# Kernel tuning notes

Measured on AMD Instinct MI355X. Metric: run time of the kernel, lower is better.

Reference implementation:

```python
import jax, jax.numpy as jnp
import numpy as np

N_BLOCKS = 16
BLOCK_SIZE = 512
TOP_K = N_BLOCKS // 4  # matches n_blocks // 4 in the source


def setup_inputs() -> dict:
    key = jax.random.key(0)
    k1, k2, k3, k4, k5 = jax.random.split(key, 5)
    in_f, out_f = 2048, 8192
    x = jax.random.normal(k1, (2, 4096, in_f), dtype=jnp.float32)
    # router: Linear(in_features, n_blocks)
    Wr = jax.random.normal(k2, (N_BLOCKS, in_f), dtype=jnp.float32) * (in_f ** -0.5)
    br = jnp.zeros((N_BLOCKS,), dtype=jnp.float32)
    # fc1: Linear(in, out); fc2: Linear(out, in). Biases are unused in the original forward.
    W1 = jax.random.normal(k3, (out_f, in_f), dtype=jnp.float32) * (in_f ** -0.5)
    W2 = jax.random.normal(k4, (in_f, out_f), dtype=jnp.float32) * (out_f ** -0.5)
    return {"x": x, "Wr": Wr, "br": br, "W1": W1, "W2": W2}


def reference(x, Wr, br, W1, W2):
    x_shape = x.shape
    in_f = x_shape[-1]
    xf = x.reshape(-1, in_f)                      # [N, in]
    n = xf.shape[0]
    # router + top-k block selection per token
    prob = jax.nn.softmax(xf @ Wr.T + br, axis=-1)          # [N, nb]
    _, idx = jax.lax.top_k(prob, TOP_K)                      # [N, k]
    mask = jnp.zeros((n, N_BLOCKS), dtype=xf.dtype)
    mask = mask.at[jnp.arange(n)[:, None], idx].set(1.0)     # [N, nb]
    # fc1 per block: h[n,i,b] = x @ W1_block_i^T  (bias never used in source)
    W1b = W1.reshape(N_BLOCKS, BLOCK_SIZE, in_f)
    h = jnp.einsum('nf,ibf->nib', xf, W1b)                   # [N, nb, bs]
    # activation, then zero out unselected blocks (unselected never reach fc2)
    h = jax.nn.gelu(h, approximate=False) * mask[:, :, None]
    # fc2 per block accumulate: y = sum_i h_i @ W2_block_i^T
    W2b = W2.reshape(in_f, N_BLOCKS, BLOCK_SIZE)
    y = jnp.einsum('nib,fib->nf', h, W2b)                    # [N, in]
    return y.reshape(x_shape)
```

## Files before the change

### kernel.cpp

```cpp
#include <hip/hip_runtime.h>
#include <hip/hip_bf16.h>

#define N_TOK 8192
#define IN_F  2048
#define OUT_F 8192
#define NB    16
#define BS    512
#define BM    128
#define MAX_MT 272

typedef short          bf16x8  __attribute__((ext_vector_type(8)));
typedef unsigned short ushort8 __attribute__((ext_vector_type(8)));
typedef float          f32x4   __attribute__((ext_vector_type(4)));
typedef _Float16       f16x8   __attribute__((ext_vector_type(8)));

#define WS_COUNTS 0
#define WS_TSTART 64
#define WS_SEL    256
#define WS_INV    (32*1024)
#define WS_LISTS  (192*1024)
#define WS_XBF    (1ull<<20)
#define WS_W1BF   (WS_XBF + 33554432ull)
#define WS_W2BF   WS_XBF
#define WS_H      (WS_XBF + 67108864ull)
#define WS_YP     (WS_H + 35651584ull)

static __device__ __forceinline__ unsigned short f2bf(float f) {
    __hip_bfloat16 h = __float2bfloat16(f);
    return *reinterpret_cast<unsigned short*>(&h);
}

static __device__ __forceinline__ void gload16(const unsigned short* g, unsigned short* lds) {
    __builtin_amdgcn_global_load_lds(
        (const __attribute__((address_space(1))) unsigned int*)g,
        (__attribute__((address_space(3))) unsigned int*)lds, 16, 0, 0);
}

__global__ __launch_bounds__(256) void router_kernel(
    const float* __restrict__ x, const float* __restrict__ Wr,
    const float* __restrict__ br, unsigned short* __restrict__ sel)
{
    const int tid = threadIdx.x;
    const int lt = tid & 63;
    const int wv = tid >> 6;
    const int tok = blockIdx.x * 4 + wv;
    const int e = lt >> 2, p = lt & 3;
    const float4* xp = (const float4*)(x + (size_t)tok * IN_F);
    const float4* wp = (const float4*)(Wr + (size_t)e * IN_F);
    double s = 0.0;
    for (int j = p; j < IN_F / 4; j += 4) {
        float4 a = xp[j], w = wp[j];
        s += (double)a.x * w.x + (double)a.y * w.y + (double)a.z * w.z + (double)a.w * w.w;
    }
    s += __shfl_down(s, 2);
    s += __shfl_down(s, 1);
    __shared__ double logits[4][NB];
    if (p == 0) logits[wv][e] = s + (double)br[e];
    __syncthreads();
    if (lt == 0) {
        unsigned used = 0, packed = 0;
        #pragma unroll
        for (int kk = 0; kk < 4; ++kk) {
            int best = 0; double bv = -1.0e300;
            #pragma unroll
            for (int i = 0; i < NB; ++i)
                if (!((used >> i) & 1u) && logits[wv][i] > bv) { bv = logits[wv][i]; best = i; }
            used |= 1u << best;
            packed |= (unsigned)best << (4 * kk);
        }
        sel[tok] = (unsigned short)packed;
    }
}

__global__ __launch_bounds__(256) void build_lists_kernel(
    const unsigned short* __restrict__ sel, int* __restrict__ counts,
    int* __restrict__ lists, unsigned* __restrict__ inv)
{
    const int e = blockIdx.x;
    const int t = threadIdx.x;
    unsigned short mysel[N_TOK / 256];
    int cnt = 0;
    #pragma unroll
    for (int i = 0; i < N_TOK / 256; ++i) {
        unsigned s = sel[i * 256 + t];
        mysel[i] = (unsigned short)s;
        bool m = ((s & 15u) == (unsigned)e) | (((s >> 4) & 15u) == (unsigned)e) |
                 (((s >> 8) & 15u) == (unsigned)e) | (((s >> 12) & 15u) == (unsigned)e);
        cnt += m ? 1 : 0;
    }
    __shared__ int ps[256];
    ps[t] = cnt;
    __syncthreads();
    #pragma unroll
    for (int off = 1; off < 256; off <<= 1) {
        int v = (t >= off) ? ps[t - off] : 0;
        __syncthreads();
        ps[t] += v;
        __syncthreads();
    }
    int pos = ps[t] - cnt;
    if (t == 255) counts[e] = ps[255];
    #pragma unroll
    for (int i = 0; i < N_TOK / 256; ++i) {
        unsigned s = mysel[i];
        bool m = ((s & 15u) == (unsigned)e) | (((s >> 4) & 15u) == (unsigned)e) |
                 (((s >> 8) & 15u) == (unsigned)e) | (((s >> 12) & 15u) == (unsigned)e);
        if (m) {
            const int tok = i * 256 + t;
            int j = ((s & 15u) == (unsigned)e) ? 0 :
                    (((s >> 4) & 15u) == (unsigned)e) ? 1 :
                    (((s >> 8) & 15u) == (unsigned)e) ? 2 : 3;
            inv[tok * 4 + j] = ((unsigned)e << 16) | (unsigned)pos;
            lists[e * N_TOK + pos++] = tok;
        }
    }
}

__global__ void scan_kernel(const int* __restrict__ counts, int* __restrict__ tstart)
{
    if (threadIdx.x == 0) {
        int acc = 0;
        for (int i = 0; i < NB; ++i) { tstart[i] = acc; acc += (counts[i] + BM - 1) / BM; }
        tstart[NB] = acc;
    }
}

__global__ __launch_bounds__(256) void convert_swz_kernel(
    const float* __restrict__ src, unsigned short* __restrict__ dst, int sh)
{
    const int total = 1 << 21;
    for (int id = blockIdx.x * 256 + threadIdx.x; id < total; id += 2048 * 256) {
        const int row = id >> sh;
        const int sr  = id & ((1 << sh) - 1);
        const int ps  = sr ^ (row & 7);
        const float4* s4 = (const float4*)(src + ((size_t)id << 3));
        float4 p0 = s4[0], p1 = s4[1];
        ushort8 o;
        o[0] = f2bf(p0.x); o[1] = f2bf(p0.y); o[2] = f2bf(p0.z); o[3] = f2bf(p0.w);
        o[4] = f2bf(p1.x); o[5] = f2bf(p1.y); o[6] = f2bf(p1.z); o[7] = f2bf(p1.w);
        *(ushort8*)(dst + (((size_t)(row) << sh) << 3) + ((size_t)ps << 3)) = o;
    }
}

__global__ __launch_bounds__(256) void fc1_kernel(
    const unsigned short* __restrict__ x_bf, const unsigned short* __restrict__ w1_bf,
    const int* __restrict__ lists, const int* __restrict__ counts,
    const int* __restrict__ tstart, unsigned short* __restrict__ h)
{
    __shared__ unsigned short As[2][BM * 64];
    __shared__ unsigned short Bs[2][BM * 64];
    const int bid = blockIdx.x;
    const int newid = (bid & 7) * 136 + (bid >> 3);
    const int nt = newid & 3, mt = newid >> 2;
    if (mt >= tstart[NB]) return;
    int b = 0;
    #pragma unroll
    for (int i = 1; i < NB; ++i) b += (mt >= tstart[i]);
    const int cnt  = counts[b];
    const int row0 = (mt - tstart[b]) * BM;
    const int tid  = threadIdx.x;
    const int wave = tid >> 6, lane = tid & 63;
    const int sr8 = lane >> 3, sph = lane & 7;

    const unsigned short* aS[4];
    const unsigned short* bS[4];
    const int loff = wave * 2048;
    #pragma unroll
    for (int t = 0; t < 4; ++t) {
        const int r = wave * 32 + t * 8 + sr8;
        const int gr = min(row0 + r, cnt - 1);
        const int tok = lists[b * N_TOK + gr];
        aS[t] = x_bf + (size_t)tok * IN_F + ((sph ^ sr8 ^ (tok & 7)) << 3);
        bS[t] = w1_bf + (size_t)(b * BS + nt * BM + r) * IN_F + (sph << 3);
    }

    const int lr16 = lane & 15, q = lane >> 4;
    const int wm = (wave >> 1) * 64, wn = (wave & 1) * 64;
    int offA[4], offB[4];
    #pragma unroll
    for (int i = 0; i < 4; ++i) {
        const int r = wm + i * 16 + lr16;
        offA[i] = r * 64 + ((q ^ (r & 7)) << 3);
    }
    #pragma unroll
    for (int j = 0; j < 4; ++j) {
        const int r = wn + j * 16 + lr16;
        offB[j] = r * 64 + ((q ^ (r & 7)) << 3);
    }

    f32x4 acc[4][4];
    #pragma unroll
    for (int i = 0; i < 4; ++i)
        #pragma unroll
        for (int j = 0; j < 4; ++j) acc[i][j] = (f32x4)0.0f;

    #pragma unroll
    for (int t = 0; t < 4; ++t) {
        gload16(aS[t], &As[0][loff + t * 512]);
        gload16(bS[t], &Bs[0][loff + t * 512]);
    }
    __syncthreads();

    const int NK = IN_F / 64;
    for (int k = 0; k < NK; ++k) {
        const int cur = k & 1;
        if (k + 1 < NK) {
            const int ko = (k + 1) * 64;
            #pragma unroll
            for (int t = 0; t < 4; ++t) {
                gload16(aS[t] + ko, &As[cur ^ 1][loff + t * 512]);
                gload16(bS[t] + ko, &Bs[cur ^ 1][loff + t * 512]);
            }
        }
        #pragma unroll
        for (int kk = 0; kk < 2; ++kk) {
            const int kx = kk << 5;
            bf16x8 a0 = *(const bf16x8*)&As[cur][offA[0] ^ kx];
            bf16x8 a1 = *(const bf16x8*)&As[cur][offA[1] ^ kx];
            bf16x8 a2 = *(const bf16x8*)&As[cur][offA[2] ^ kx];
            bf16x8 a3 = *(const bf16x8*)&As[cur][offA[3] ^ kx];
            bf16x8 b0 = *(const bf16x8*)&Bs[cur][offB[0] ^ kx];
            bf16x8 b1 = *(const bf16x8*)&Bs[cur][offB[1] ^ kx];
            bf16x8 b2 = *(const bf16x8*)&Bs[cur][offB[2] ^ kx];
            bf16x8 b3 = *(const bf16x8*)&Bs[cur][offB[3] ^ kx];
            acc[0][0] = __builtin_amdgcn_mfma_f32_16x16x32_bf16(a0, b0, acc[0][0], 0, 0, 0);
            acc[0][1] = __builtin_amdgcn_mfma_f32_16x16x32_bf16(a0, b1, acc[0][1], 0, 0, 0);
            acc[0][2] = __builtin_amdgcn_mfma_f32_16x16x32_bf16(a0, b2, acc[0][2], 0, 0, 0);
            acc[0][3] = __builtin_amdgcn_mfma_f32_16x16x32_bf16(a0, b3, acc[0][3], 0, 0, 0);
            acc[1][0] = __builtin_amdgcn_mfma_f32_16x16x32_bf16(a1, b0, acc[1][0], 0, 0, 0);
            acc[1][1] = __builtin_amdgcn_mfma_f32_16x16x32_bf16(a1, b1, acc[1][1], 0, 0, 0);
            acc[1][2] = __builtin_amdgcn_mfma_f32_16x16x32_bf16(a1, b2, acc[1][2], 0, 0, 0);
            acc[1][3] = __builtin_amdgcn_mfma_f32_16x16x32_bf16(a1, b3, acc[1][3], 0, 0, 0);
            acc[2][0] = __builtin_amdgcn_mfma_f32_16x16x32_bf16(a2, b0, acc[2][0], 0, 0, 0);
            acc[2][1] = __builtin_amdgcn_mfma_f32_16x16x32_bf16(a2, b1, acc[2][1], 0, 0, 0);
            acc[2][2] = __builtin_amdgcn_mfma_f32_16x16x32_bf16(a2, b2, acc[2][2], 0, 0, 0);
            acc[2][3] = __builtin_amdgcn_mfma_f32_16x16x32_bf16(a2, b3, acc[2][3], 0, 0, 0);
            acc[3][0] = __builtin_amdgcn_mfma_f32_16x16x32_bf16(a3, b0, acc[3][0], 0, 0, 0);
            acc[3][1] = __builtin_amdgcn_mfma_f32_16x16x32_bf16(a3, b1, acc[3][1], 0, 0, 0);
            acc[3][2] = __builtin_amdgcn_mfma_f32_16x16x32_bf16(a3, b2, acc[3][2], 0, 0, 0);
            acc[3][3] = __builtin_amdgcn_mfma_f32_16x16x32_bf16(a3, b3, acc[3][3], 0, 0, 0);
        }
        __syncthreads();
    }
    #pragma unroll
    for (int i = 0; i < 4; ++i) {
        #pragma unroll
        for (int r = 0; r < 4; ++r) {
            const int lrow = wm + i * 16 + q * 4 + r;
            if (row0 + lrow < cnt) {
                const size_t hrow = (size_t)(mt * BM + lrow) * BS;
                const int r7 = (lrow & 7) << 3;
                #pragma unroll
                for (int j = 0; j < 4; ++j) {
                    const int col = nt * BM + wn + j * 16 + lr16;
                    float v = acc[i][j][r];
                    v = 0.5f * v * (1.0f + erff(v * 0.70710678118654752f));
                    h[hrow + (col ^ r7)] = f2bf(v);
                }
            }
        }
    }
}

__global__ __launch_bounds__(256) void fc2_kernel(
    const unsigned short* __restrict__ h, const unsigned short* __restrict__ w2_bf,
    const int* __restrict__ counts, const int* __restrict__ tstart,
    _Float16* __restrict__ yp)
{
    __shared__ unsigned short As[2][BM * 64];
    __shared__ unsigned short Bs[2][BM * 64];
    const int bid = blockIdx.x;
    const int newid = (bid & 7) * 544 + (bid >> 3);
    const int nt = newid & 15, mt = newid >> 4;
    if (mt >= tstart[NB]) return;
    int b = 0;
    #pragma unroll
    for (int i = 1; i < NB; ++i) b += (mt >= tstart[i]);
    const int cnt  = counts[b];
    const int row0 = (mt - tstart[b]) * BM;
    const int tid  = threadIdx.x;
    const int wave = tid >> 6, lane = tid & 63;
    const int sr8 = lane >> 3, sph = lane & 7;

    const unsigned short* aS[4];
    const unsigned short* bS[4];
    const int loff = wave * 2048;
    #pragma unroll
    for (int t = 0; t < 4; ++t) {
        const int r = wave * 32 + t * 8 + sr8;
        aS[t] = h + (size_t)(mt * BM + r) * BS + (sph << 3);
        bS[t] = w2_bf + (size_t)(nt * BM + r) * OUT_F + b * BS + (sph << 3);
    }

    const int lr16 = lane & 15, q = lane >> 4;
    const int wm = (wave >> 1) * 64, wn = (wave & 1) * 64;
    int offA[4], offB[4];
    #pragma unroll
    for (int i = 0; i < 4; ++i) {
        const int r = wm + i * 16 + lr16;
        offA[i] = r * 64 + ((q ^ (r & 7)) << 3);
    }
    #pragma unroll
    for (int j = 0; j < 4; ++j) {
        const int r = wn + j * 16 + lr16;
        offB[j] = r * 64 + ((q ^ (r & 7)) << 3);
    }

    f32x4 acc[4][4];
    #pragma unroll
    for (int i = 0; i < 4; ++i)
        #pragma unroll
        for (int j = 0; j < 4; ++j) acc[i][j] = (f32x4)0.0f;

    #pragma unroll
    for (int t = 0; t < 4; ++t) {
        gload16(aS[t], &As[0][loff + t * 512]);
        gload16(bS[t], &Bs[0][loff + t * 512]);
    }
    __syncthreads();

    const int NK = BS / 64;
    for (int k = 0; k < NK; ++k) {
        const int cur = k & 1;
        if (k + 1 < NK) {
            const int ko = (k + 1) * 64;
            #pragma unroll
            for (int t = 0; t < 4; ++t) {
                gload16(aS[t] + ko, &As[cur ^ 1][loff + t * 512]);
                gload16(bS[t] + ko, &Bs[cur ^ 1][loff + t * 512]);
            }
        }
        #pragma unroll
        for (int kk = 0; kk < 2; ++kk) {
            const int kx = kk << 5;
            bf16x8 a0 = *(const bf16x8*)&As[cur][offA[0] ^ kx];
            bf16x8 a1 = *(const bf16x8*)&As[cur][offA[1] ^ kx];
            bf16x8 a2 = *(const bf16x8*)&As[cur][offA[2] ^ kx];
            bf16x8 a3 = *(const bf16x8*)&As[cur][offA[3] ^ kx];
            bf16x8 b0 = *(const bf16x8*)&Bs[cur][offB[0] ^ kx];
            bf16x8 b1 = *(const bf16x8*)&Bs[cur][offB[1] ^ kx];
            bf16x8 b2 = *(const bf16x8*)&Bs[cur][offB[2] ^ kx];
            bf16x8 b3 = *(const bf16x8*)&Bs[cur][offB[3] ^ kx];
            acc[0][0] = __builtin_amdgcn_mfma_f32_16x16x32_bf16(a0, b0, acc[0][0], 0, 0, 0);
            acc[0][1] = __builtin_amdgcn_mfma_f32_16x16x32_bf16(a0, b1, acc[0][1], 0, 0, 0);
            acc[0][2] = __builtin_amdgcn_mfma_f32_16x16x32_bf16(a0, b2, acc[0][2], 0, 0, 0);
            acc[0][3] = __builtin_amdgcn_mfma_f32_16x16x32_bf16(a0, b3, acc[0][3], 0, 0, 0);
            acc[1][0] = __builtin_amdgcn_mfma_f32_16x16x32_bf16(a1, b0, acc[1][0], 0, 0, 0);
            acc[1][1] = __builtin_amdgcn_mfma_f32_16x16x32_bf16(a1, b1, acc[1][1], 0, 0, 0);
            acc[1][2] = __builtin_amdgcn_mfma_f32_16x16x32_bf16(a1, b2, acc[1][2], 0, 0, 0);
            acc[1][3] = __builtin_amdgcn_mfma_f32_16x16x32_bf16(a1, b3, acc[1][3], 0, 0, 0);
            acc[2][0] = __builtin_amdgcn_mfma_f32_16x16x32_bf16(a2, b0, acc[2][0], 0, 0, 0);
            acc[2][1] = __builtin_amdgcn_mfma_f32_16x16x32_bf16(a2, b1, acc[2][1], 0, 0, 0);
            acc[2][2] = __builtin_amdgcn_mfma_f32_16x16x32_bf16(a2, b2, acc[2][2], 0, 0, 0);
            acc[2][3] = __builtin_amdgcn_mfma_f32_16x16x32_bf16(a2, b3, acc[2][3], 0, 0, 0);
            acc[3][0] = __builtin_amdgcn_mfma_f32_16x16x32_bf16(a3, b0, acc[3][0], 0, 0, 0);
            acc[3][1] = __builtin_amdgcn_mfma_f32_16x16x32_bf16(a3, b1, acc[3][1], 0, 0, 0);
            acc[3][2] = __builtin_amdgcn_mfma_f32_16x16x32_bf16(a3, b2, acc[3][2], 0, 0, 0);
            acc[3][3] = __builtin_amdgcn_mfma_f32_16x16x32_bf16(a3, b3, acc[3][3], 0, 0, 0);
        }
        __syncthreads();
    }
    #pragma unroll
    for (int i = 0; i < 4; ++i) {
        #pragma unroll
        for (int r = 0; r < 4; ++r) {
            const int lrow = wm + i * 16 + q * 4 + r;
            if (row0 + lrow < cnt) {
                _Float16* yrow = yp + (size_t)(mt * BM + lrow) * IN_F + nt * BM + wn + lr16;
                #pragma unroll
                for (int j = 0; j < 4; ++j)
                    yrow[j * 16] = (_Float16)acc[i][j][r];
            }
        }
    }
}

__global__ __launch_bounds__(256) void reduce_kernel(
    const _Float16* __restrict__ yp, const unsigned* __restrict__ inv,
    const int* __restrict__ tstart, float* __restrict__ y)
{
    const int tok = blockIdx.x;
    __shared__ size_t rbase[4];
    if (threadIdx.x < 4) {
        unsigned v = inv[tok * 4 + threadIdx.x];
        rbase[threadIdx.x] = (size_t)(tstart[v >> 16] * BM + (int)(v & 0xFFFFu)) * IN_F;
    }
    __syncthreads();
    const int c = threadIdx.x * 8;
    f16x8 v0 = *(const f16x8*)(yp + rbase[0] + c);
    f16x8 v1 = *(const f16x8*)(yp + rbase[1] + c);
    f16x8 v2 = *(const f16x8*)(yp + rbase[2] + c);
    f16x8 v3 = *(const f16x8*)(yp + rbase[3] + c);
    float out[8];
    #pragma unroll
    for (int j = 0; j < 8; ++j)
        out[j] = (float)v0[j] + (float)v1[j] + (float)v2[j] + (float)v3[j];
    float4* yo = (float4*)(y + (size_t)tok * IN_F + c);
    yo[0] = make_float4(out[0], out[1], out[2], out[3]);
    yo[1] = make_float4(out[4], out[5], out[6], out[7]);
}

extern "C" void kernel_launch(void* const* d_in, const int* in_sizes, int n_in,
                              void* d_out, int out_size, void* d_ws, size_t ws_size,
                              hipStream_t stream) {
    const float* x  = (const float*)d_in[0];
    const float* Wr = (const float*)d_in[1];
    const float* br = (const float*)d_in[2];
    const float* W1 = (const float*)d_in[3];
    const float* W2 = (const float*)d_in[4];
    float* y = (float*)d_out;
    char* ws = (char*)d_ws;
    int* counts = (int*)(ws + WS_COUNTS);
    int* tstart = (int*)(ws + WS_TSTART);
    unsigned short* sel = (unsigned short*)(ws + WS_SEL);
    unsigned* inv = (unsigned*)(ws + WS_INV);
    int* lists  = (int*)(ws + WS_LISTS);
    unsigned short* x_bf  = (unsigned short*)(ws + WS_XBF);
    unsigned short* w1_bf = (unsigned short*)(ws + WS_W1BF);
    unsigned short* w2_bf = (unsigned short*)(ws + WS_W2BF);
    unsigned short* h     = (unsigned short*)(ws + WS_H);
    _Float16* yp          = (_Float16*)(ws + WS_YP);

    hipLaunchKernelGGL(router_kernel, dim3(N_TOK / 4), dim3(256), 0, stream, x, Wr, br, sel);
    hipLaunchKernelGGL(build_lists_kernel, dim3(NB), dim3(256), 0, stream, sel, counts, lists, inv);
    hipLaunchKernelGGL(scan_kernel, dim3(1), dim3(64), 0, stream, counts, tstart);
    hipLaunchKernelGGL(convert_swz_kernel, dim3(2048), dim3(256), 0, stream, x,  x_bf,  8);
    hipLaunchKernelGGL(convert_swz_kernel, dim3(2048), dim3(256), 0, stream, W1, w1_bf, 8);
    hipLaunchKernelGGL(fc1_kernel, dim3(4 * MAX_MT), dim3(256), 0, stream, x_bf, w1_bf, lists, counts, tstart, h);
    hipLaunchKernelGGL(convert_swz_kernel, dim3(2048), dim3(256), 0, stream, W2, w2_bf, 10);
    hipLaunchKernelGGL(fc2_kernel, dim3(16 * MAX_MT), dim3(256), 0, stream, h, w2_bf, counts, tstart, yp);
    hipLaunchKernelGGL(reduce_kernel, dim3(N_TOK), dim3(256), 0, stream, yp, inv, tstart, y);
}
```

Baseline: 453.0 us.

## Replace full syncthreads with partial vmcnt waits and raw barriers in GEMM loops

```diff
diff --git a/kernel.cpp b/kernel.cpp
--- a/kernel.cpp
+++ b/kernel.cpp
@@ -35,6 +35,24 @@
         (const __attribute__((address_space(1))) unsigned int*)g,
         (__attribute__((address_space(3))) unsigned int*)lds, 16, 0, 0);
 }
+
+#define MFMA16(ai, bi) \
+    acc[0][0] = __builtin_amdgcn_mfma_f32_16x16x32_bf16(ai##0, bi##0, acc[0][0], 0, 0, 0); \
+    acc[0][1] = __builtin_amdgcn_mfma_f32_16x16x32_bf16(ai##0, bi##1, acc[0][1], 0, 0, 0); \
+    acc[0][2] = __builtin_amdgcn_mfma_f32_16x16x32_bf16(ai##0, bi##2, acc[0][2], 0, 0, 0); \
+    acc[0][3] = __builtin_amdgcn_mfma_f32_16x16x32_bf16(ai##0, bi##3, acc[0][3], 0, 0, 0); \
+    acc[1][0] = __builtin_amdgcn_mfma_f32_16x16x32_bf16(ai##1, bi##0, acc[1][0], 0, 0, 0); \
+    acc[1][1] = __builtin_amdgcn_mfma_f32_16x16x32_bf16(ai##1, bi##1, acc[1][1], 0, 0, 0); \
+    acc[1][2] = __builtin_amdgcn_mfma_f32_16x16x32_bf16(ai##1, bi##2, acc[1][2], 0, 0, 0); \
+    acc[1][3] = __builtin_amdgcn_mfma_f32_16x16x32_bf16(ai##1, bi##3, acc[1][3], 0, 0, 0); \
+    acc[2][0] = __builtin_amdgcn_mfma_f32_16x16x32_bf16(ai##2, bi##0, acc[2][0], 0, 0, 0); \
+    acc[2][1] = __builtin_amdgcn_mfma_f32_16x16x32_bf16(ai##2, bi##1, acc[2][1], 0, 0, 0); \
+    acc[2][2] = __builtin_amdgcn_mfma_f32_16x16x32_bf16(ai##2, bi##2, acc[2][2], 0, 0, 0); \
+    acc[2][3] = __builtin_amdgcn_mfma_f32_16x16x32_bf16(ai##2, bi##3, acc[2][3], 0, 0, 0); \
+    acc[3][0] = __builtin_amdgcn_mfma_f32_16x16x32_bf16(ai##3, bi##0, acc[3][0], 0, 0, 0); \
+    acc[3][1] = __builtin_amdgcn_mfma_f32_16x16x32_bf16(ai##3, bi##1, acc[3][1], 0, 0, 0); \
+    acc[3][2] = __builtin_amdgcn_mfma_f32_16x16x32_bf16(ai##3, bi##2, acc[3][2], 0, 0, 0); \
+    acc[3][3] = __builtin_amdgcn_mfma_f32_16x16x32_bf16(ai##3, bi##3, acc[3][3], 0, 0, 0);
 
 __global__ __launch_bounds__(256) void router_kernel(
     const float* __restrict__ x, const float* __restrict__ Wr,
@@ -199,7 +217,6 @@
         gload16(aS[t], &As[0][loff + t * 512]);
         gload16(bS[t], &Bs[0][loff + t * 512]);
     }
-    __syncthreads();
 
     const int NK = IN_F / 64;
     for (int k = 0; k < NK; ++k) {
@@ -211,36 +228,32 @@
                 gload16(aS[t] + ko, &As[cur ^ 1][loff + t * 512]);
                 gload16(bS[t] + ko, &Bs[cur ^ 1][loff + t * 512]);
             }
-        }
-        #pragma unroll
-        for (int kk = 0; kk < 2; ++kk) {
-            const int kx = kk << 5;
-            bf16x8 a0 = *(const bf16x8*)&As[cur][offA[0] ^ kx];
-            bf16x8 a1 = *(const bf16x8*)&As[cur][offA[1] ^ kx];
-            bf16x8 a2 = *(const bf16x8*)&As[cur][offA[2] ^ kx];
-            bf16x8 a3 = *(const bf16x8*)&As[cur][offA[3] ^ kx];
-            bf16x8 b0 = *(const bf16x8*)&Bs[cur][offB[0] ^ kx];
-            bf16x8 b1 = *(const bf16x8*)&Bs[cur][offB[1] ^ kx];
-            bf16x8 b2 = *(const bf16x8*)&Bs[cur][offB[2] ^ kx];
-            bf16x8 b3 = *(const bf16x8*)&Bs[cur][offB[3] ^ kx];
-            acc[0][0] = __builtin_amdgcn_mfma_f32_16x16x32_bf16(a0, b0, acc[0][0], 0, 0, 0);
-            acc[0][1] = __builtin_amdgcn_mfma_f32_16x16x32_bf16(a0, b1, acc[0][1], 0, 0, 0);
-            acc[0][2] = __builtin_amdgcn_mfma_f32_16x16x32_bf16(a0, b2, acc[0][2], 0, 0, 0);
-            acc[0][3] = __builtin_amdgcn_mfma_f32_16x16x32_bf16(a0, b3, acc[0][3], 0, 0, 0);
-            acc[1][0] = __builtin_amdgcn_mfma_f32_16x16x32_bf16(a1, b0, acc[1][0], 0, 0, 0);
-            acc[1][1] = __builtin_amdgcn_mfma_f32_16x16x32_bf16(a1, b1, acc[1][1], 0, 0, 0);
-            acc[1][2] = __builtin_amdgcn_mfma_f32_16x16x32_bf16(a1, b2, acc[1][2], 0, 0, 0);
-            acc[1][3] = __builtin_amdgcn_mfma_f32_16x16x32_bf16(a1, b3, acc[1][3], 0, 0, 0);
-            acc[2][0] = __builtin_amdgcn_mfma_f32_16x16x32_bf16(a2, b0, acc[2][0], 0, 0, 0);
-            acc[2][1] = __builtin_amdgcn_mfma_f32_16x16x32_bf16(a2, b1, acc[2][1], 0, 0, 0);
-            acc[2][2] = __builtin_amdgcn_mfma_f32_16x16x32_bf16(a2, b2, acc[2][2], 0, 0, 0);
-            acc[2][3] = __builtin_amdgcn_mfma_f32_16x16x32_bf16(a2, b3, acc[2][3], 0, 0, 0);
-            acc[3][0] = __builtin_amdgcn_mfma_f32_16x16x32_bf16(a3, b0, acc[3][0], 0, 0, 0);
-            acc[3][1] = __builtin_amdgcn_mfma_f32_16x16x32_bf16(a3, b1, acc[3][1], 0, 0, 0);
-            acc[3][2] = __builtin_amdgcn_mfma_f32_16x16x32_bf16(a3, b2, acc[3][2], 0, 0, 0);
-            acc[3][3] = __builtin_amdgcn_mfma_f32_16x16x32_bf16(a3, b3, acc[3][3], 0, 0, 0);
-        }
-        __syncthreads();
+            asm volatile("s_waitcnt vmcnt(8)" ::: "memory");
+        } else {
+            asm volatile("s_waitcnt vmcnt(0)" ::: "memory");
+        }
+        __builtin_amdgcn_s_barrier();
+        __builtin_amdgcn_sched_barrier(0);
+        {
+            bf16x8 a0, a1, a2, a3, b0, b1, b2, b3;
+            #pragma unroll
+            for (int kk = 0; kk < 2; ++kk) {
+                const int kx = kk << 5;
+                a0 = *(const bf16x8*)&As[cur][offA[0] ^ kx];
+                a1 = *(const bf16x8*)&As[cur][offA[1] ^ kx];
+                a2 = *(const bf16x8*)&As[cur][offA[2] ^ kx];
+                a3 = *(const bf16x8*)&As[cur][offA[3] ^ kx];
+                b0 = *(const bf16x8*)&Bs[cur][offB[0] ^ kx];
+                b1 = *(const bf16x8*)&Bs[cur][offB[1] ^ kx];
+                b2 = *(const bf16x8*)&Bs[cur][offB[2] ^ kx];
+                b3 = *(const bf16x8*)&Bs[cur][offB[3] ^ kx];
+                __builtin_amdgcn_s_setprio(1);
+                MFMA16(a, b)
+                __builtin_amdgcn_s_setprio(0);
+            }
+        }
+        __builtin_amdgcn_sched_barrier(0);
+        __builtin_amdgcn_s_barrier();
     }
     #pragma unroll
     for (int i = 0; i < 4; ++i) {
@@ -317,7 +330,6 @@
         gload16(aS[t], &As[0][loff + t * 512]);
         gload16(bS[t], &Bs[0][loff + t * 512]);
     }
-    __syncthreads();
 
     const int NK = BS / 64;
     for (int k = 0; k < NK; ++k) {
@@ -329,36 +341,32 @@
                 gload16(aS[t] + ko, &As[cur ^ 1][loff + t * 512]);
                 gload16(bS[t] + ko, &Bs[cur ^ 1][loff + t * 512]);
             }
-        }
-        #pragma unroll
-        for (int kk = 0; kk < 2; ++kk) {
-            const int kx = kk << 5;
-            bf16x8 a0 = *(const bf16x8*)&As[cur][offA[0] ^ kx];
-            bf16x8 a1 = *(const bf16x8*)&As[cur][offA[1] ^ kx];
-            bf16x8 a2 = *(const bf16x8*)&As[cur][offA[2] ^ kx];
-            bf16x8 a3 = *(const bf16x8*)&As[cur][offA[3] ^ kx];
-            bf16x8 b0 = *(const bf16x8*)&Bs[cur][offB[0] ^ kx];
-            bf16x8 b1 = *(const bf16x8*)&Bs[cur][offB[1] ^ kx];
-            bf16x8 b2 = *(const bf16x8*)&Bs[cur][offB[2] ^ kx];
-            bf16x8 b3 = *(const bf16x8*)&Bs[cur][offB[3] ^ kx];
-            acc[0][0] = __builtin_amdgcn_mfma_f32_16x16x32_bf16(a0, b0, acc[0][0], 0, 0, 0);
-            acc[0][1] = __builtin_amdgcn_mfma_f32_16x16x32_bf16(a0, b1, acc[0][1], 0, 0, 0);
-            acc[0][2] = __builtin_amdgcn_mfma_f32_16x16x32_bf16(a0, b2, acc[0][2], 0, 0, 0);
-            acc[0][3] = __builtin_amdgcn_mfma_f32_16x16x32_bf16(a0, b3, acc[0][3], 0, 0, 0);
-            acc[1][0] = __builtin_amdgcn_mfma_f32_16x16x32_bf16(a1, b0, acc[1][0], 0, 0, 0);
-            acc[1][1] = __builtin_amdgcn_mfma_f32_16x16x32_bf16(a1, b1, acc[1][1], 0, 0, 0);
-            acc[1][2] = __builtin_amdgcn_mfma_f32_16x16x32_bf16(a1, b2, acc[1][2], 0, 0, 0);
-            acc[1][3] = __builtin_amdgcn_mfma_f32_16x16x32_bf16(a1, b3, acc[1][3], 0, 0, 0);
-            acc[2][0] = __builtin_amdgcn_mfma_f32_16x16x32_bf16(a2, b0, acc[2][0], 0, 0, 0);
-            acc[2][1] = __builtin_amdgcn_mfma_f32_16x16x32_bf16(a2, b1, acc[2][1], 0, 0, 0);
-            acc[2][2] = __builtin_amdgcn_mfma_f32_16x16x32_bf16(a2, b2, acc[2][2], 0, 0, 0);
-            acc[2][3] = __builtin_amdgcn_mfma_f32_16x16x32_bf16(a2, b3, acc[2][3], 0, 0, 0);
-            acc[3][0] = __builtin_amdgcn_mfma_f32_16x16x32_bf16(a3, b0, acc[3][0], 0, 0, 0);
-            acc[3][1] = __builtin_amdgcn_mfma_f32_16x16x32_bf16(a3, b1, acc[3][1], 0, 0, 0);
-            acc[3][2] = __builtin_amdgcn_mfma_f32_16x16x32_bf16(a3, b2, acc[3][2], 0, 0, 0);
-            acc[3][3] = __builtin_amdgcn_mfma_f32_16x16x32_bf16(a3, b3, acc[3][3], 0, 0, 0);
-        }
-        __syncthreads();
+            asm volatile("s_waitcnt vmcnt(8)" ::: "memory");
+        } else {
+            asm volatile("s_waitcnt vmcnt(0)" ::: "memory");
+        }
+        __builtin_amdgcn_s_barrier();
+        __builtin_amdgcn_sched_barrier(0);
+        {
+            bf16x8 a0, a1, a2, a3, b0, b1, b2, b3;
+            #pragma unroll
+            for (int kk = 0; kk < 2; ++kk) {
+                const int kx = kk << 5;
+                a0 = *(const bf16x8*)&As[cur][offA[0] ^ kx];
+                a1 = *(const bf16x8*)&As[cur][offA[1] ^ kx];
+                a2 = *(const bf16x8*)&As[cur][offA[2] ^ kx];
+                a3 = *(const bf16x8*)&As[cur][offA[3] ^ kx];
+                b0 = *(const bf16x8*)&Bs[cur][offB[0] ^ kx];
+                b1 = *(const bf16x8*)&Bs[cur][offB[1] ^ kx];
+                b2 = *(const bf16x8*)&Bs[cur][offB[2] ^ kx];
+                b3 = *(const bf16x8*)&Bs[cur][offB[3] ^ kx];
+                __builtin_amdgcn_s_setprio(1);
+                MFMA16(a, b)
+                __builtin_amdgcn_s_setprio(0);
+            }
+        }
+        __builtin_amdgcn_sched_barrier(0);
+        __builtin_amdgcn_s_barrier();
     }
     #pragma unroll
     for (int i = 0; i < 4; ++i) {
```

Result: faster. 430.4 us (-5.0%).

## Load A operand directly from global into registers, keep only B in LDS

Applied to the files above, without the earlier changes.

```diff
diff --git a/kernel.cpp b/kernel.cpp
--- a/kernel.cpp
+++ b/kernel.cpp
@@ -125,14 +125,14 @@
     }
 }
 
-__global__ __launch_bounds__(256) void convert_swz_kernel(
-    const float* __restrict__ src, unsigned short* __restrict__ dst, int sh)
+__global__ __launch_bounds__(256) void convert_kernel(
+    const float* __restrict__ src, unsigned short* __restrict__ dst, int sh, int swz)
 {
     const int total = 1 << 21;
     for (int id = blockIdx.x * 256 + threadIdx.x; id < total; id += 2048 * 256) {
         const int row = id >> sh;
         const int sr  = id & ((1 << sh) - 1);
-        const int ps  = sr ^ (row & 7);
+        const int ps  = swz ? (sr ^ (row & 7)) : sr;
         const float4* s4 = (const float4*)(src + ((size_t)id << 3));
         float4 p0 = s4[0], p1 = s4[1];
         ushort8 o;
@@ -142,12 +142,33 @@
     }
 }
 
+#define LDA(dst, ke) \
+    { _Pragma("unroll") for (int i = 0; i < 4; ++i) { \
+        dst##0[i] = *(const bf16x8*)(aP[i] + (ke)); \
+        dst##1[i] = *(const bf16x8*)(aP[i] + (ke) + 32); } }
+
+#define STB(ke, buf) \
+    { _Pragma("unroll") for (int g = 0; g < 4; ++g) \
+        gload16(bS[g] + (ke), &Bs[buf][(wave << 11) + (g << 9)]); }
+
+#define COMP(buf, ar) \
+    { _Pragma("unroll") for (int hf = 0; hf < 2; ++hf) { \
+        bf16x8 b0 = *(const bf16x8*)&Bs[buf][offB[0] ^ (hf << 5)]; \
+        bf16x8 b1 = *(const bf16x8*)&Bs[buf][offB[1] ^ (hf << 5)]; \
+        bf16x8 b2 = *(const bf16x8*)&Bs[buf][offB[2] ^ (hf << 5)]; \
+        bf16x8 b3 = *(const bf16x8*)&Bs[buf][offB[3] ^ (hf << 5)]; \
+        bf16x8* av = hf ? ar##1 : ar##0; \
+        _Pragma("unroll") for (int i = 0; i < 4; ++i) { \
+            acc[i][0] = __builtin_amdgcn_mfma_f32_16x16x32_bf16(av[i], b0, acc[i][0], 0, 0, 0); \
+            acc[i][1] = __builtin_amdgcn_mfma_f32_16x16x32_bf16(av[i], b1, acc[i][1], 0, 0, 0); \
+            acc[i][2] = __builtin_amdgcn_mfma_f32_16x16x32_bf16(av[i], b2, acc[i][2], 0, 0, 0); \
+            acc[i][3] = __builtin_amdgcn_mfma_f32_16x16x32_bf16(av[i], b3, acc[i][3], 0, 0, 0); } } }
+
 __global__ __launch_bounds__(256) void fc1_kernel(
     const unsigned short* __restrict__ x_bf, const unsigned short* __restrict__ w1_bf,
     const int* __restrict__ lists, const int* __restrict__ counts,
     const int* __restrict__ tstart, unsigned short* __restrict__ h)
 {
-    __shared__ unsigned short As[2][BM * 64];
     __shared__ unsigned short Bs[2][BM * 64];
     const int bid = blockIdx.x;
     const int newid = (bid & 7) * 136 + (bid >> 3);
@@ -160,28 +181,22 @@
     const int row0 = (mt - tstart[b]) * BM;
     const int tid  = threadIdx.x;
     const int wave = tid >> 6, lane = tid & 63;
-    const int sr8 = lane >> 3, sph = lane & 7;
-
-    const unsigned short* aS[4];
-    const unsigned short* bS[4];
-    const int loff = wave * 2048;
-    #pragma unroll
-    for (int t = 0; t < 4; ++t) {
-        const int r = wave * 32 + t * 8 + sr8;
-        const int gr = min(row0 + r, cnt - 1);
-        const int tok = lists[b * N_TOK + gr];
-        aS[t] = x_bf + (size_t)tok * IN_F + ((sph ^ sr8 ^ (tok & 7)) << 3);
-        bS[t] = w1_bf + (size_t)(b * BS + nt * BM + r) * IN_F + (sph << 3);
-    }
-
     const int lr16 = lane & 15, q = lane >> 4;
     const int wm = (wave >> 1) * 64, wn = (wave & 1) * 64;
-    int offA[4], offB[4];
+
+    const unsigned short* aP[4];
     #pragma unroll
     for (int i = 0; i < 4; ++i) {
-        const int r = wm + i * 16 + lr16;
-        offA[i] = r * 64 + ((q ^ (r & 7)) << 3);
-    }
+        const int gr = min(row0 + wm + i * 16 + lr16, cnt - 1);
+        aP[i] = x_bf + (size_t)lists[b * N_TOK + gr] * IN_F + q * 8;
+    }
+    const unsigned short* bS[4];
+    #pragma unroll
+    for (int g = 0; g < 4; ++g) {
+        const int rg = wave * 32 + g * 8 + (lane >> 3);
+        bS[g] = w1_bf + (size_t)(b * BS + nt * BM + rg) * IN_F + (lane & 7) * 8;
+    }
+    int offB[4];
     #pragma unroll
     for (int j = 0; j < 4; ++j) {
         const int r = wn + j * 16 + lr16;
@@ -194,53 +209,17 @@
         #pragma unroll
         for (int j = 0; j < 4; ++j) acc[i][j] = (f32x4)0.0f;
 
-    #pragma unroll
-    for (int t = 0; t < 4; ++t) {
-        gload16(aS[t], &As[0][loff + t * 512]);
-        gload16(bS[t], &Bs[0][loff + t * 512]);
-    }
-    __syncthreads();
+    bf16x8 aE0[4], aE1[4], aO0[4], aO1[4];
+    STB(0, 0); LDA(aE, 0);
 
     const int NK = IN_F / 64;
-    for (int k = 0; k < NK; ++k) {
-        const int cur = k & 1;
-        if (k + 1 < NK) {
-            const int ko = (k + 1) * 64;
-            #pragma unroll
-            for (int t = 0; t < 4; ++t) {
-                gload16(aS[t] + ko, &As[cur ^ 1][loff + t * 512]);
-                gload16(bS[t] + ko, &Bs[cur ^ 1][loff + t * 512]);
-            }
-        }
-        #pragma unroll
-        for (int kk = 0; kk < 2; ++kk) {
-            const int kx = kk << 5;
-            bf16x8 a0 = *(const bf16x8*)&As[cur][offA[0] ^ kx];
-            bf16x8 a1 = *(const bf16x8*)&As[cur][offA[1] ^ kx];
-            bf16x8 a2 = *(const bf16x8*)&As[cur][offA[2] ^ kx];
-            bf16x8 a3 = *(const bf16x8*)&As[cur][offA[3] ^ kx];
-            bf16x8 b0 = *(const bf16x8*)&Bs[cur][offB[0] ^ kx];
-            bf16x8 b1 = *(const bf16x8*)&Bs[cur][offB[1] ^ kx];
-            bf16x8 b2 = *(const bf16x8*)&Bs[cur][offB[2] ^ kx];
-            bf16x8 b3 = *(const bf16x8*)&Bs[cur][offB[3] ^ kx];
-            acc[0][0] = __builtin_amdgcn_mfma_f32_16x16x32_bf16(a0, b0, acc[0][0], 0, 0, 0);
-            acc[0][1] = __builtin_amdgcn_mfma_f32_16x16x32_bf16(a0, b1, acc[0][1], 0, 0, 0);
-            acc[0][2] = __builtin_amdgcn_mfma_f32_16x16x32_bf16(a0, b2, acc[0][2], 0, 0, 0);
-            acc[0][3] = __builtin_amdgcn_mfma_f32_16x16x32_bf16(a0, b3, acc[0][3], 0, 0, 0);
-            acc[1][0] = __builtin_amdgcn_mfma_f32_16x16x32_bf16(a1, b0, acc[1][0], 0, 0, 0);
-            acc[1][1] = __builtin_amdgcn_mfma_f32_16x16x32_bf16(a1, b1, acc[1][1], 0, 0, 0);
-            acc[1][2] = __builtin_amdgcn_mfma_f32_16x16x32_bf16(a1, b2, acc[1][2], 0, 0, 0);
-            acc[1][3] = __builtin_amdgcn_mfma_f32_16x16x32_bf16(a1, b3, acc[1][3], 0, 0, 0);
-            acc[2][0] = __builtin_amdgcn_mfma_f32_16x16x32_bf16(a2, b0, acc[2][0], 0, 0, 0);
-            acc[2][1] = __builtin_amdgcn_mfma_f32_16x16x32_bf16(a2, b1, acc[2][1], 0, 0, 0);
-            acc[2][2] = __builtin_amdgcn_mfma_f32_16x16x32_bf16(a2, b2, acc[2][2], 0, 0, 0);
-            acc[2][3] = __builtin_amdgcn_mfma_f32_16x16x32_bf16(a2, b3, acc[2][3], 0, 0, 0);
-            acc[3][0] = __builtin_amdgcn_mfma_f32_16x16x32_bf16(a3, b0, acc[3][0], 0, 0, 0);
-            acc[3][1] = __builtin_amdgcn_mfma_f32_16x16x32_bf16(a3, b1, acc[3][1], 0, 0, 0);
-            acc[3][2] = __builtin_amdgcn_mfma_f32_16x16x32_bf16(a3, b2, acc[3][2], 0, 0, 0);
-            acc[3][3] = __builtin_amdgcn_mfma_f32_16x16x32_bf16(a3, b3, acc[3][3], 0, 0, 0);
-        }
-        __syncthreads();
+    for (int k = 0; k < NK; k += 2) {
+        __syncthreads();
+        if (k + 1 < NK) { STB((k + 1) * 64, 1); LDA(aO, (k + 1) * 64); }
+        COMP(0, aE)
+        __syncthreads();
+        if (k + 2 < NK) { STB((k + 2) * 64, 0); LDA(aE, (k + 2) * 64); }
+        COMP(1, aO)
     }
     #pragma unroll
     for (int i = 0; i < 4; ++i) {
@@ -249,13 +228,11 @@
             const int lrow = wm + i * 16 + q * 4 + r;
             if (row0 + lrow < cnt) {
                 const size_t hrow = (size_t)(mt * BM + lrow) * BS;
-                const int r7 = (lrow & 7) << 3;
                 #pragma unroll
                 for (int j = 0; j < 4; ++j) {
-                    const int col = nt * BM + wn + j * 16 + lr16;
                     float v = acc[i][j][r];
                     v = 0.5f * v * (1.0f + erff(v * 0.70710678118654752f));
-                    h[hrow + (col ^ r7)] = f2bf(v);
+                    h[hrow + nt * BM + wn + j * 16 + lr16] = f2bf(v);
                 }
             }
         }
@@ -267,7 +244,6 @@
     const int* __restrict__ counts, const int* __restrict__ tstart,
     _Float16* __restrict__ yp)
 {
-    __shared__ unsigned short As[2][BM * 64];
     __shared__ unsigned short Bs[2][BM * 64];
     const int bid = blockIdx.x;
     const int newid = (bid & 7) * 544 + (bid >> 3);
@@ -280,26 +256,20 @@
     const int row0 = (mt - tstart[b]) * BM;
     const int tid  = threadIdx.x;
     const int wave = tid >> 6, lane = tid & 63;
-    const int sr8 = lane >> 3, sph = lane & 7;
-
-    const unsigned short* aS[4];
-    const unsigned short* bS[4];
-    const int loff = wave * 2048;
-    #pragma unroll
-    for (int t = 0; t < 4; ++t) {
-        const int r = wave * 32 + t * 8 + sr8;
-        aS[t] = h + (size_t)(mt * BM + r) * BS + (sph << 3);
-        bS[t] = w2_bf + (size_t)(nt * BM + r) * OUT_F + b * BS + (sph << 3);
-    }
-
     const int lr16 = lane & 15, q = lane >> 4;
     const int wm = (wave >> 1) * 64, wn = (wave & 1) * 64;
-    int offA[4], offB[4];
-    #pragma unroll
-    for (int i = 0; i < 4; ++i) {
-        const int r = wm + i * 16 + lr16;
-        offA[i] = r * 64 + ((q ^ (r & 7)) << 3);
-    }
+
+    const unsigned short* aP[4];
+    #pragma unroll
+    for (int i = 0; i < 4; ++i)
+        aP[i] = h + (size_t)(mt * BM + wm + i * 16 + lr16) * BS + q * 8;
+    const unsigned short* bS[4];
+    #pragma unroll
+    for (int g = 0; g < 4; ++g) {
+        const int rg = wave * 32 + g * 8 + (lane >> 3);
+        bS[g] = w2_bf + (size_t)(nt * BM + rg) * OUT_F + b * BS + (lane & 7) * 8;
+    }
+    int offB[4];
     #pragma unroll
     for (int j = 0; j < 4; ++j) {
         const int r = wn + j * 16 + lr16;
@@ -312,53 +282,17 @@
         #pragma unroll
         for (int j = 0; j < 4; ++j) acc[i][j] = (f32x4)0.0f;
 
-    #pragma unroll
-    for (int t = 0; t < 4; ++t) {
-        gload16(aS[t], &As[0][loff + t * 512]);
-        gload16(bS[t], &Bs[0][loff + t * 512]);
-    }
-    __syncthreads();
+    bf16x8 aE0[4], aE1[4], aO0[4], aO1[4];
+    STB(0, 0); LDA(aE, 0);
 
     const int NK = BS / 64;
-    for (int k = 0; k < NK; ++k) {
-        const int cur = k & 1;
-        if (k + 1 < NK) {
-            const int ko = (k + 1) * 64;
-            #pragma unroll
-            for (int t = 0; t < 4; ++t) {
-                gload16(aS[t] + ko, &As[cur ^ 1][loff + t * 512]);
-                gload16(bS[t] + ko, &Bs[cur ^ 1][loff + t * 512]);
-            }
-        }
-        #pragma unroll
-        for (int kk = 0; kk < 2; ++kk) {
-            const int kx = kk << 5;
-            bf16x8 a0 = *(const bf16x8*)&As[cur][offA[0] ^ kx];
-            bf16x8 a1 = *(const bf16x8*)&As[cur][offA[1] ^ kx];
-            bf16x8 a2 = *(const bf16x8*)&As[cur][offA[2] ^ kx];
-            bf16x8 a3 = *(const bf16x8*)&As[cur][offA[3] ^ kx];
-            bf16x8 b0 = *(const bf16x8*)&Bs[cur][offB[0] ^ kx];
-            bf16x8 b1 = *(const bf16x8*)&Bs[cur][offB[1] ^ kx];
-            bf16x8 b2 = *(const bf16x8*)&Bs[cur][offB[2] ^ kx];
-            bf16x8 b3 = *(const bf16x8*)&Bs[cur][offB[3] ^ kx];
-            acc[0][0] = __builtin_amdgcn_mfma_f32_16x16x32_bf16(a0, b0, acc[0][0], 0, 0, 0);
-            acc[0][1] = __builtin_amdgcn_mfma_f32_16x16x32_bf16(a0, b1, acc[0][1], 0, 0, 0);
-            acc[0][2] = __builtin_amdgcn_mfma_f32_16x16x32_bf16(a0, b2, acc[0][2], 0, 0, 0);
-            acc[0][3] = __builtin_amdgcn_mfma_f32_16x16x32_bf16(a0, b3, acc[0][3], 0, 0, 0);
-            acc[1][0] = __builtin_amdgcn_mfma_f32_16x16x32_bf16(a1, b0, acc[1][0], 0, 0, 0);
-            acc[1][1] = __builtin_amdgcn_mfma_f32_16x16x32_bf16(a1, b1, acc[1][1], 0, 0, 0);
-            acc[1][2] = __builtin_amdgcn_mfma_f32_16x16x32_bf16(a1, b2, acc[1][2], 0, 0, 0);
-            acc[1][3] = __builtin_amdgcn_mfma_f32_16x16x32_bf16(a1, b3, acc[1][3], 0, 0, 0);
-            acc[2][0] = __builtin_amdgcn_mfma_f32_16x16x32_bf16(a2, b0, acc[2][0], 0, 0, 0);
-            acc[2][1] = __builtin_amdgcn_mfma_f32_16x16x32_bf16(a2, b1, acc[2][1], 0, 0, 0);
-            acc[2][2] = __builtin_amdgcn_mfma_f32_16x16x32_bf16(a2, b2, acc[2][2], 0, 0, 0);
-            acc[2][3] = __builtin_amdgcn_mfma_f32_16x16x32_bf16(a2, b3, acc[2][3], 0, 0, 0);
-            acc[3][0] = __builtin_amdgcn_mfma_f32_16x16x32_bf16(a3, b0, acc[3][0], 0, 0, 0);
-            acc[3][1] = __builtin_amdgcn_mfma_f32_16x16x32_bf16(a3, b1, acc[3][1], 0, 0, 0);
-            acc[3][2] = __builtin_amdgcn_mfma_f32_16x16x32_bf16(a3, b2, acc[3][2], 0, 0, 0);
-            acc[3][3] = __builtin_amdgcn_mfma_f32_16x16x32_bf16(a3, b3, acc[3][3], 0, 0, 0);
-        }
-        __syncthreads();
+    for (int k = 0; k < NK; k += 2) {
+        __syncthreads();
+        if (k + 1 < NK) { STB((k + 1) * 64, 1); LDA(aO, (k + 1) * 64); }
+        COMP(0, aE)
+        __syncthreads();
+        if (k + 2 < NK) { STB((k + 2) * 64, 0); LDA(aE, (k + 2) * 64); }
+        COMP(1, aO)
     }
     #pragma unroll
     for (int i = 0; i < 4; ++i) {
@@ -424,10 +358,10 @@
     hipLaunchKernelGGL(router_kernel, dim3(N_TOK / 4), dim3(256), 0, stream, x, Wr, br, sel);
     hipLaunchKernelGGL(build_lists_kernel, dim3(NB), dim3(256), 0, stream, sel, counts, lists, inv);
     hipLaunchKernelGGL(scan_kernel, dim3(1), dim3(64), 0, stream, counts, tstart);
-    hipLaunchKernelGGL(convert_swz_kernel, dim3(2048), dim3(256), 0, stream, x,  x_bf,  8);
-    hipLaunchKernelGGL(convert_swz_kernel, dim3(2048), dim3(256), 0, stream, W1, w1_bf, 8);
+    hipLaunchKernelGGL(convert_kernel, dim3(2048), dim3(256), 0, stream, x,  x_bf,  8, 0);
+    hipLaunchKernelGGL(convert_kernel, dim3(2048), dim3(256), 0, stream, W1, w1_bf, 8, 1);
     hipLaunchKernelGGL(fc1_kernel, dim3(4 * MAX_MT), dim3(256), 0, stream, x_bf, w1_bf, lists, counts, tstart, h);
-    hipLaunchKernelGGL(convert_swz_kernel, dim3(2048), dim3(256), 0, stream, W2, w2_bf, 10);
+    hipLaunchKernelGGL(convert_kernel, dim3(2048), dim3(256), 0, stream, W2, w2_bf, 10, 1);
     hipLaunchKernelGGL(fc2_kernel, dim3(16 * MAX_MT), dim3(256), 0, stream, h, w2_bf, counts, tstart, yp);
     hipLaunchKernelGGL(reduce_kernel, dim3(N_TOK), dim3(256), 0, stream, yp, inv, tstart, y);
 }
```

Result: slower. 535.2 us (+18.1%).
